# Kernel optimization log

Measured on AMD Instinct MI355X. Metric: run time of the kernel, lower is better.

Reference implementation:

```python
import jax, jax.numpy as jnp
import numpy as np

MARGIN = 0.5
EPSILON = 0.1
LAMBDA_ORDER = 1.0
LAMBDA_CAUSALITY = 0.8
LAMBDA_TRANSITIVITY = 0.6
LOG_CLAMP = -100.0  # torch BCELoss clamps log outputs at -100


def setup_inputs() -> dict:
    key = jax.random.key(0)
    k1, k2, k3, k4, k5 = jax.random.split(key, 5)
    B, S = 4, 2048
    pred_times = jax.random.normal(k1, (B, S), dtype=jnp.float32)
    pred_causal = jax.random.uniform(k2, (B, S, S), dtype=jnp.float32)
    target_times = jax.random.normal(k3, (B, S), dtype=jnp.float32)
    target_causal = jax.random.randint(k4, (B, S, S), 0, 2).astype(jnp.int32)
    target_precedence = jax.random.randint(k5, (B, S, S), 0, 2).astype(jnp.int32)
    return {
        'pred_times': pred_times,
        'pred_causal': pred_causal,
        'target_times': target_times,
        'target_causal': target_causal,
        'target_precedence': target_precedence,
    }


def reference(pred_times, pred_causal, target_times, target_causal, target_precedence):
    B, S = pred_times.shape

    # --- ordering loss ---
    # time_diff[b,i,j] = pred_times[b,i] - pred_times[b,j]
    time_diff = pred_times[:, :, None] - pred_times[:, None, :]
    target_order = (target_times[:, :, None] < target_times[:, None, :]).astype(pred_times.dtype)
    ordering_loss = jnp.mean(jax.nn.relu(MARGIN - time_diff * target_order))

    # --- causality loss (BCE, matching torch.nn.BCELoss log clamping) ---
    t = target_causal.astype(pred_causal.dtype)
    log_p = jnp.maximum(jnp.log(pred_causal), LOG_CLAMP)
    log_1mp = jnp.maximum(jnp.log1p(-pred_causal), LOG_CLAMP)
    causality_loss = -jnp.mean(t * log_p + (1.0 - t) * log_1mp)

    # --- transitivity loss ---
    # Original triple loop: for i<j<k, if precedence[0,i,k]>0 add
    # mean_b relu(eps - (pt[:,k]-pt[:,i])). The body depends only on (i,k);
    # j contributes multiplicity (k-i-1). Collapse to a weighted pair sum.
    idx = jnp.arange(S)
    gap = idx[None, :] - idx[:, None]              # k - i
    mult = jnp.where(gap >= 2, gap - 1, 0).astype(pred_times.dtype)  # (k-i-1) for k>=i+2
    w = mult * (target_precedence[0] > 0).astype(pred_times.dtype)   # [S,S]
    # violation[b,i,k] = relu(eps - (pred_times[b,k] - pred_times[b,i]))
    violation = jax.nn.relu(EPSILON - (pred_times[:, None, :] - pred_times[:, :, None]))
    trans_sum = jnp.sum(w * jnp.mean(violation, axis=0))
    denom = max(1, S * (S - 1) * (S - 2) / 6)
    transitivity_loss = trans_sum / jnp.asarray(denom, dtype=pred_times.dtype)

    total_loss = (LAMBDA_ORDER * ordering_loss
                  + LAMBDA_CAUSALITY * causality_loss
                  + LAMBDA_TRANSITIVITY * transitivity_loss)
    return ordering_loss, causality_loss, transitivity_loss, total_loss
```

## Files before the change

### kernel.cpp

```cpp
#include <hip/hip_runtime.h>

#define S 2048
#define BB 4
#define NQUAD (S * S / 4)
#define BLOCK 256
#define QT 4
#define NBLOCKS (NQUAD / (BLOCK * QT))

__global__ __launch_bounds__(BLOCK, 2) void tcl_main(
    const float* __restrict__ pred_times,
    const float* __restrict__ pred_causal,
    const float* __restrict__ target_times,
    const int*   __restrict__ target_causal,
    const int*   __restrict__ target_prec,
    float* __restrict__ partials)
{
    const int t = threadIdx.x;
    const int qbase = blockIdx.x * (BLOCK * QT) + t;

    int4   prec[QT];
    float4 pc[QT][BB];
    int4   tc[QT][BB];
    int    ii[QT], jj[QT];

#pragma unroll
    for (int n = 0; n < QT; ++n) {
        const int q  = qbase + n * BLOCK;
        const int i  = q >> 9;
        const int j0 = (q & 511) << 2;
        ii[n] = i; jj[n] = j0;
        prec[n] = *(const int4*)(target_prec + (size_t)i * S + j0);
#pragma unroll
        for (int b = 0; b < BB; ++b) {
            const size_t rb = (size_t)b * S * S + (size_t)i * S + j0;
            pc[n][b] = *(const float4*)(pred_causal + rb);
            tc[n][b] = *(const int4*)(target_causal + rb);
        }
    }

    float ord = 0.f, bce = 0.f, trans = 0.f;

#pragma unroll
    for (int n = 0; n < QT; ++n) {
        const int i = ii[n], j0 = jj[n];
        const int pv[4] = {prec[n].x, prec[n].y, prec[n].z, prec[n].w};
        float w[4];
#pragma unroll
        for (int l = 0; l < 4; ++l) {
            const int gap = (j0 + l) - i;
            w[l] = (pv[l] > 0 && gap >= 2) ? (float)(gap - 1) : 0.f;
        }

#pragma unroll
        for (int b = 0; b < BB; ++b) {
            const float  pti = pred_times[b * S + i];
            const float  tti = target_times[b * S + i];
            const float4 ptj = *(const float4*)(pred_times + b * S + j0);
            const float4 ttj = *(const float4*)(target_times + b * S + j0);

            const float ptjl[4] = {ptj.x, ptj.y, ptj.z, ptj.w};
            const float ttjl[4] = {ttj.x, ttj.y, ttj.z, ttj.w};
            const float pcl[4]  = {pc[n][b].x, pc[n][b].y, pc[n][b].z, pc[n][b].w};
            const int   tcl[4]  = {tc[n][b].x, tc[n][b].y, tc[n][b].z, tc[n][b].w};

#pragma unroll
            for (int l = 0; l < 4; ++l) {
                ord += (tti < ttjl[l]) ? fmaxf(0.5f - (pti - ptjl[l]), 0.f) : 0.5f;
                const float x = (tcl[l] != 0) ? pcl[l] : (1.f - pcl[l]);
                bce -= fmaxf(__logf(x), -100.f);
                trans += w[l] * fmaxf(0.1f - (ptjl[l] - pti), 0.f);
            }
        }
    }

#pragma unroll
    for (int off = 32; off > 0; off >>= 1) {
        ord   += __shfl_down(ord, off);
        bce   += __shfl_down(bce, off);
        trans += __shfl_down(trans, off);
    }

    __shared__ float s_o[BLOCK / 64], s_c[BLOCK / 64], s_t[BLOCK / 64];
    const int lane = t & 63;
    const int wv   = t >> 6;
    if (lane == 0) { s_o[wv] = ord; s_c[wv] = bce; s_t[wv] = trans; }
    __syncthreads();
    if (t == 0) {
        float o = 0.f, c = 0.f, tr = 0.f;
#pragma unroll
        for (int k = 0; k < BLOCK / 64; ++k) { o += s_o[k]; c += s_c[k]; tr += s_t[k]; }
        partials[blockIdx.x]               = o;
        partials[NBLOCKS + blockIdx.x]     = c;
        partials[2 * NBLOCKS + blockIdx.x] = tr;
    }
}

__global__ __launch_bounds__(BLOCK) void tcl_finalize(
    const float* __restrict__ partials, float* __restrict__ out)
{
    const int t = threadIdx.x;
    float o = 0.f, c = 0.f, tr = 0.f;
    for (int k = t; k < NBLOCKS; k += BLOCK) {
        o  += partials[k];
        c  += partials[NBLOCKS + k];
        tr += partials[2 * NBLOCKS + k];
    }
#pragma unroll
    for (int off = 32; off > 0; off >>= 1) {
        o  += __shfl_down(o, off);
        c  += __shfl_down(c, off);
        tr += __shfl_down(tr, off);
    }
    __shared__ float s_o[BLOCK / 64], s_c[BLOCK / 64], s_t[BLOCK / 64];
    const int lane = t & 63;
    const int wv   = t >> 6;
    if (lane == 0) { s_o[wv] = o; s_c[wv] = c; s_t[wv] = tr; }
    __syncthreads();
    if (t == 0) {
        float so = 0.f, sc = 0.f, st = 0.f;
#pragma unroll
        for (int k = 0; k < BLOCK / 64; ++k) { so += s_o[k]; sc += s_c[k]; st += s_t[k]; }
        const double cnt   = (double)BB * S * S;
        const double denom = 2048.0 * 2047.0 * 2046.0 / 6.0;
        const float ordm = (float)((double)so / cnt);
        const float bcem = (float)((double)sc / cnt);
        const float trm  = (float)((double)st / (double)BB / denom);
        out[0] = ordm;
        out[1] = bcem;
        out[2] = trm;
        out[3] = 1.0f * ordm + 0.8f * bcem + 0.6f * trm;
    }
}

extern "C" void kernel_launch(void* const* d_in, const int* in_sizes, int n_in,
                              void* d_out, int out_size, void* d_ws, size_t ws_size,
                              hipStream_t stream) {
    const float* pred_times    = (const float*)d_in[0];
    const float* pred_causal   = (const float*)d_in[1];
    const float* target_times  = (const float*)d_in[2];
    const int*   target_causal = (const int*)d_in[3];
    const int*   target_prec   = (const int*)d_in[4];
    float* out      = (float*)d_out;
    float* partials = (float*)d_ws;

    tcl_main<<<dim3(NBLOCKS), dim3(BLOCK), 0, stream>>>(
        pred_times, pred_causal, target_times, target_causal, target_prec, partials);
    tcl_finalize<<<dim3(1), dim3(BLOCK), 0, stream>>>(partials, out);
}
```

Measured before the change: 195.3 us.

## Decouple pairwise ordering/transitivity work from streaming BCE across separate block ranges

Splits the fused kernel so the first 512 blocks handle the per-(i,j) ordering and transitivity terms, while all 4096 blocks stream the BCE over the flat pred_causal/target_causal arrays with a grid-stride layout. The old version kept 32 float4/int4 loads live per thread, which limited occupancy to 2 blocks per CU. The new BCE loop needs far fewer registers, so launch bounds are raised to 6 blocks per CU, meant to give more memory-level parallelism on what is a bandwidth-bound stream of roughly 130 MB. The cost is load imbalance: the first 512 blocks carry extra compute and loads. The finalize kernel now reduces 4096 partials instead of 1024.

```diff
diff --git a/kernel.cpp b/kernel.cpp
--- a/kernel.cpp
+++ b/kernel.cpp
@@ -2,12 +2,15 @@
 
 #define S 2048
 #define BB 4
-#define NQUAD (S * S / 4)
 #define BLOCK 256
-#define QT 4
-#define NBLOCKS (NQUAD / (BLOCK * QT))
+#define NB_TOTAL 4096
+#define NB_TR 512
+#define NQ_BCE (BB * S * S / 4)
+#define NQ_TR  (S * S / 4)
+#define BCE_ITERS (NQ_BCE / (NB_TOTAL * BLOCK))
+#define TR_ITERS  (NQ_TR / (NB_TR * BLOCK))
 
-__global__ __launch_bounds__(BLOCK, 2) void tcl_main(
+__global__ __launch_bounds__(BLOCK, 6) void tcl_main(
     const float* __restrict__ pred_times,
     const float* __restrict__ pred_causal,
     const float* __restrict__ target_times,
@@ -15,60 +18,57 @@
     const int*   __restrict__ target_prec,
     float* __restrict__ partials)
 {
-    const int t = threadIdx.x;
-    const int qbase = blockIdx.x * (BLOCK * QT) + t;
+    const int t   = threadIdx.x;
+    const int bid = blockIdx.x;
 
-    int4   prec[QT];
-    float4 pc[QT][BB];
-    int4   tc[QT][BB];
-    int    ii[QT], jj[QT];
+    float ord = 0.f, bce = 0.f, trans = 0.f;
 
+    if (bid < NB_TR) {
+        const int base = bid * BLOCK + t;
 #pragma unroll
-    for (int n = 0; n < QT; ++n) {
-        const int q  = qbase + n * BLOCK;
-        const int i  = q >> 9;
-        const int j0 = (q & 511) << 2;
-        ii[n] = i; jj[n] = j0;
-        prec[n] = *(const int4*)(target_prec + (size_t)i * S + j0);
+        for (int it = 0; it < TR_ITERS; ++it) {
+            const int q  = base + it * (NB_TR * BLOCK);
+            const int i  = q >> 9;
+            const int j0 = (q & 511) << 2;
+            const int4 prec = *(const int4*)(target_prec + (size_t)i * S + j0);
+            const int pv[4] = {prec.x, prec.y, prec.z, prec.w};
+            float w[4];
 #pragma unroll
-        for (int b = 0; b < BB; ++b) {
-            const size_t rb = (size_t)b * S * S + (size_t)i * S + j0;
-            pc[n][b] = *(const float4*)(pred_causal + rb);
-            tc[n][b] = *(const int4*)(target_causal + rb);
+            for (int l = 0; l < 4; ++l) {
+                const int gap = (j0 + l) - i;
+                w[l] = (pv[l] > 0 && gap >= 2) ? (float)(gap - 1) : 0.f;
+            }
+#pragma unroll
+            for (int b = 0; b < BB; ++b) {
+                const float  pti = pred_times[b * S + i];
+                const float  tti = target_times[b * S + i];
+                const float4 ptj = *(const float4*)(pred_times + b * S + j0);
+                const float4 ttj = *(const float4*)(target_times + b * S + j0);
+                const float ptjl[4] = {ptj.x, ptj.y, ptj.z, ptj.w};
+                const float ttjl[4] = {ttj.x, ttj.y, ttj.z, ttj.w};
+#pragma unroll
+                for (int l = 0; l < 4; ++l) {
+                    const float diff = pti - ptjl[l];
+                    ord   += (tti < ttjl[l]) ? fmaxf(0.5f - diff, 0.f) : 0.5f;
+                    trans += w[l] * fmaxf(0.1f + diff, 0.f);
+                }
+            }
         }
     }
 
-    float ord = 0.f, bce = 0.f, trans = 0.f;
-
+    {
+        const size_t base = (size_t)bid * BLOCK + t;
 #pragma unroll
-    for (int n = 0; n < QT; ++n) {
-        const int i = ii[n], j0 = jj[n];
-        const int pv[4] = {prec[n].x, prec[n].y, prec[n].z, prec[n].w};
-        float w[4];
-#pragma unroll
-        for (int l = 0; l < 4; ++l) {
-            const int gap = (j0 + l) - i;
-            w[l] = (pv[l] > 0 && gap >= 2) ? (float)(gap - 1) : 0.f;
-        }
-
-#pragma unroll
-        for (int b = 0; b < BB; ++b) {
-            const float  pti = pred_times[b * S + i];
-            const float  tti = target_times[b * S + i];
-            const float4 ptj = *(const float4*)(pred_times + b * S + j0);
-            const float4 ttj = *(const float4*)(target_times + b * S + j0);
-
-            const float ptjl[4] = {ptj.x, ptj.y, ptj.z, ptj.w};
-            const float ttjl[4] = {ttj.x, ttj.y, ttj.z, ttj.w};
-            const float pcl[4]  = {pc[n][b].x, pc[n][b].y, pc[n][b].z, pc[n][b].w};
-            const int   tcl[4]  = {tc[n][b].x, tc[n][b].y, tc[n][b].z, tc[n][b].w};
-
+        for (int it = 0; it < BCE_ITERS; ++it) {
+            const size_t q = base + (size_t)it * ((size_t)NB_TOTAL * BLOCK);
+            const float4 pc = *(const float4*)(pred_causal + q * 4);
+            const int4   tc = *(const int4*)(target_causal + q * 4);
+            const float pcl[4] = {pc.x, pc.y, pc.z, pc.w};
+            const int   tcl[4] = {tc.x, tc.y, tc.z, tc.w};
 #pragma unroll
             for (int l = 0; l < 4; ++l) {
-                ord += (tti < ttjl[l]) ? fmaxf(0.5f - (pti - ptjl[l]), 0.f) : 0.5f;
                 const float x = (tcl[l] != 0) ? pcl[l] : (1.f - pcl[l]);
                 bce -= fmaxf(__logf(x), -100.f);
-                trans += w[l] * fmaxf(0.1f - (ptjl[l] - pti), 0.f);
             }
         }
     }
@@ -79,7 +79,6 @@
         bce   += __shfl_down(bce, off);
         trans += __shfl_down(trans, off);
     }
-
     __shared__ float s_o[BLOCK / 64], s_c[BLOCK / 64], s_t[BLOCK / 64];
     const int lane = t & 63;
     const int wv   = t >> 6;
@@ -89,9 +88,9 @@
         float o = 0.f, c = 0.f, tr = 0.f;
 #pragma unroll
         for (int k = 0; k < BLOCK / 64; ++k) { o += s_o[k]; c += s_c[k]; tr += s_t[k]; }
-        partials[blockIdx.x]               = o;
-        partials[NBLOCKS + blockIdx.x]     = c;
-        partials[2 * NBLOCKS + blockIdx.x] = tr;
+        partials[bid]                = o;
+        partials[NB_TOTAL + bid]     = c;
+        partials[2 * NB_TOTAL + bid] = tr;
     }
 }
 
@@ -100,10 +99,10 @@
 {
     const int t = threadIdx.x;
     float o = 0.f, c = 0.f, tr = 0.f;
-    for (int k = t; k < NBLOCKS; k += BLOCK) {
+    for (int k = t; k < NB_TOTAL; k += BLOCK) {
         o  += partials[k];
-        c  += partials[NBLOCKS + k];
-        tr += partials[2 * NBLOCKS + k];
+        c  += partials[NB_TOTAL + k];
+        tr += partials[2 * NB_TOTAL + k];
     }
 #pragma unroll
     for (int off = 32; off > 0; off >>= 1) {
@@ -143,7 +142,7 @@
     float* out      = (float*)d_out;
     float* partials = (float*)d_ws;
 
-    tcl_main<<<dim3(NBLOCKS), dim3(BLOCK), 0, stream>>>(
+    tcl_main<<<dim3(NB_TOTAL), dim3(BLOCK), 0, stream>>>(
         pred_times, pred_causal, target_times, target_causal, target_prec, partials);
     tcl_finalize<<<dim3(1), dim3(BLOCK), 0, stream>>>(partials, out);
 }
```

After: 191.5 us. 1.02x faster.
